# Performance work log

Hardware: AMD Instinct MI355X
Metric: run time of the kernel (lower is better)

Reference implementation:

```python
import jax, jax.numpy as jnp
import numpy as np

PAD = 1
THRESH = 10.0


def setup_inputs() -> dict:
    key = jax.random.key(0)
    k1, k2, k3 = jax.random.split(key, 3)
    x = jax.random.normal(k1, (8, 16, 62, 62), dtype=jnp.float32)
    W = jax.random.normal(k2, (32, 16, 3, 3), dtype=jnp.float32)
    b = jax.random.normal(k3, (32,), dtype=jnp.float32)
    return {"x": x, "W": W, "b": b}


def reference(x, W, b):
    # ZeroPad2d(padding) on all four sides
    x = jnp.pad(x, ((0, 0), (0, 0), (PAD, PAD), (PAD, PAD)))
    T, C, xr, xc = x.shape
    O, _, wr, wc = W.shape
    L = xr * xc

    # get_xfft_thresh: 1D FFT over flattened HxW, zero coeffs with |Re| < thresh
    xf = jnp.fft.fft(x.reshape(T, C, L))                      # (T,C,L) complex
    xf = jnp.where(jnp.abs(xf.real) < THRESH, jnp.zeros_like(xf), xf)

    # get_Wfft: zero-pad kernel to (xr,xc) bottom/right, flatten, reverse along
    # length (flipud(flip([0,1])) nets to a flip of the last axis only), then FFT
    Wp = jnp.pad(W, ((0, 0), (0, 0), (0, xr - wr), (0, xc - wc))).reshape(O, C, L)
    Wf = jnp.fft.fft(Wp[:, :, ::-1])                          # (O,C,L) complex

    # fftConv1D, batched over (image, out_channel):
    y = jnp.fft.ifft(xf[:, None, :, :] * Wf[None, :, :, :]).real  # (T,O,C,L)
    # torch.roll(y, 1) with no dims rolls the FLATTENED (C*L) tensor by 1
    y = jnp.roll(y.reshape(T, O, C * L), 1, axis=-1).reshape(T, O, C, xr, xc)
    y = y.sum(axis=2)                                         # sum over in-channels
    ans_r, ans_c = xr - wr + 1, xc - wc + 1
    y = y[:, :, :ans_r, :ans_c]
    return y + b[None, :, None, None]
```

## Files before the change

### kernel.cpp

```cpp
#include <hip/hip_runtime.h>
#include <math.h>

#define TWO_PI 6.28318530717958647692f
#define NT     1024
#define RPW    4
#define PITCH  65
#define THRESH 10.0f
#define C128   0.998795456205172393f
#define S128   0.049067674327418015f

typedef float v2f __attribute__((ext_vector_type(2)));

__device__ __forceinline__ int brev6(int x) {
    return (int)(__brev((unsigned)x) >> 26);
}

__device__ __forceinline__ v2f cmul_add(v2f a, v2f b, v2f acc) {
    acc += (v2f){a.x, a.x} * b;
    acc += (v2f){a.y, a.y} * (v2f){-b.y, b.x};
    return acc;
}

struct Tw6 { v2f t[6]; };

__device__ __forceinline__ Tw6 make_tw6(int lane, float sign) {
    Tw6 T;
    #pragma unroll
    for (int s = 0; s < 6; ++s) {
        int h = 1 << s;
        int j = lane & (h - 1);
        float ang = sign * (TWO_PI / 64.0f) * (float)(j * (32 >> s));
        float c, si;
        __sincosf(ang, &si, &c);
        T.t[s] = (v2f){c, si};
    }
    return T;
}

template<int R>
__device__ __forceinline__ void fft64_dif_t(float (&re)[R], float (&im)[R],
                                            int lane, const Tw6& T) {
    #pragma unroll
    for (int s = 5; s >= 0; --s) {
        const int h = 1 << s;
        float wr = T.t[s].x, wi = T.t[s].y;
        bool upper = (lane & h) != 0;
        float cwr = upper ? wr : 1.0f;
        float cwi = upper ? wi : 0.0f;
        float sgn = upper ? -1.0f : 1.0f;
        #pragma unroll
        for (int m = 0; m < R; ++m) {
            float orr = __shfl_xor(re[m], h, 64);
            float oii = __shfl_xor(im[m], h, 64);
            float ar = fmaf(sgn, re[m], orr);
            float ai = fmaf(sgn, im[m], oii);
            re[m] = ar * cwr - ai * cwi;
            im[m] = ar * cwi + ai * cwr;
        }
    }
}

template<int R>
__device__ __forceinline__ void fft64_dit_t(float (&re)[R], float (&im)[R],
                                            int lane, const Tw6& T) {
    #pragma unroll
    for (int s = 0; s < 6; ++s) {
        const int h = 1 << s;
        float wr = T.t[s].x, wi = T.t[s].y;
        bool upper = (lane & h) != 0;
        float cwr = upper ? wr : 1.0f;
        float cwi = upper ? wi : 0.0f;
        float sgn = upper ? -1.0f : 1.0f;
        #pragma unroll
        for (int m = 0; m < R; ++m) {
            float tr = re[m] * cwr - im[m] * cwi;
            float ti = re[m] * cwi + im[m] * cwr;
            float orr = __shfl_xor(tr, h, 64);
            float oii = __shfl_xor(ti, h, 64);
            re[m] = fmaf(sgn, tr, orr);
            im[m] = fmaf(sgn, ti, oii);
        }
    }
}

__global__ __launch_bounds__(NT) void fwd_kernel(const float* __restrict__ x,
                                                 float2* __restrict__ X) {
    __shared__ float sre[64 * PITCH];
    __shared__ float sim[64 * PITCH];
    const int task = blockIdx.x;
    const int tid  = threadIdx.x;
    const int lane = tid & 63;
    const int w    = tid >> 6;
    const float* xr = x + (size_t)task * 62 * 62;

    for (int idx = tid; idx < 4096; idx += NT) {
        int r = idx >> 6, s = idx & 63;
        float v = 0.0f;
        if (r >= 1 && r <= 62 && s >= 1 && s <= 62)
            v = xr[(r - 1) * 62 + (s - 1)];
        sre[r * PITCH + s] = v;
    }
    __syncthreads();

    const Tw6 Tf = make_tw6(lane, -1.0f);

    float re[RPW], im[RPW];
    #pragma unroll
    for (int m = 0; m < RPW; ++m) {
        re[m] = sre[lane * PITCH + (w * RPW + m)];
        im[m] = 0.0f;
    }
    fft64_dif_t<RPW>(re, im, lane, Tf);
    const int k1 = brev6(lane);
    #pragma unroll
    for (int m = 0; m < RPW; ++m) {
        int n2 = w * RPW + m;
        float cr, ci;
        __sincosf(-(TWO_PI / 4096.0f) * (float)(k1 * n2), &ci, &cr);
        float rr = re[m] * cr - im[m] * ci;
        im[m]    = re[m] * ci + im[m] * cr;
        re[m]    = rr;
    }
    __syncthreads();
    #pragma unroll
    for (int m = 0; m < RPW; ++m) {
        int n2 = w * RPW + m;
        sre[k1 * PITCH + n2] = re[m];
        sim[k1 * PITCH + n2] = im[m];
    }
    __syncthreads();

    float rb[3], ib[3];
    const int rows[3] = {2 * w, 2 * w + 1, 32};
    #pragma unroll
    for (int s = 0; s < 3; ++s) {
        rb[s] = sre[rows[s] * PITCH + lane];
        ib[s] = sim[rows[s] * PITCH + lane];
    }
    fft64_dif_t<3>(rb, ib, lane, Tf);
    float2* Xrow = X + (size_t)task * 4096;
    #pragma unroll
    for (int s = 0; s < 3; ++s) {
        if (s < 2 || w == 0) {
            float rr = rb[s], ii = ib[s];
            if (fabsf(rr) < THRESH) { rr = 0.0f; ii = 0.0f; }
            Xrow[rows[s] * 64 + lane] = make_float2(rr, ii);
        }
    }
}

__global__ __launch_bounds__(NT, 4) void conv_kernel(const float2* __restrict__ X,
                                                     const float* __restrict__ W,
                                                     const float* __restrict__ b,
                                                     float* __restrict__ out) {
    __shared__ float sre[64 * PITCH];
    __shared__ float sim[64 * PITCH];
    const int t    = blockIdx.x >> 5;
    const int o    = blockIdx.x & 31;
    const int tid  = threadIdx.x;
    const int lane = tid & 63;
    const int w    = tid >> 6;

    const int k2 = brev6(lane);
    float elr, eli;
    __sincosf((TWO_PI / 64.0f) * (float)k2, &eli, &elr);

    const Tw6 Ti = make_tw6(lane, +1.0f);

    const int rA = 2 * w, rB = 2 * w + 1;
    float uAr, uAi, vAr, vAi, uBr, uBi, vBr, vBi;
    __sincosf((TWO_PI / 64.0f) * (float)rA, &uAi, &uAr);
    __sincosf((TWO_PI / 4096.0f) * (float)rA, &vAi, &vAr);
    __sincosf((TWO_PI / 64.0f) * (float)rB, &uBi, &uBr);
    __sincosf((TWO_PI / 4096.0f) * (float)rB, &vBi, &vBr);
    v2f uA = {uAr, uAi};
    v2f vA = {vAr * elr - vAi * eli, vAr * eli + vAi * elr};
    v2f v2A = {vA.x * vA.x - vA.y * vA.y, 2.0f * vA.x * vA.y};
    v2f uB = {uBr, uBi};
    v2f vB = {vBr * elr - vBi * eli, vBr * eli + vBi * elr};
    v2f v2B = {vB.x * vB.x - vB.y * vB.y, 2.0f * vB.x * vB.y};
    v2f vC = {C128 * elr - S128 * eli, C128 * eli + S128 * elr};
    v2f v2C = {vC.x * vC.x - vC.y * vC.y, 2.0f * vC.x * vC.y};

    v2f SA = {0,0}, SB = {0,0}, SC = {0,0};

    const float2* Xt = X + (size_t)t * 16 * 4096 + lane;
    const float*  wo = W + o * 144;

    v2f xA[4], xB[4], xC[4];
    #pragma unroll
    for (int j = 0; j < 4; ++j) {
        { float2 q = Xt[j * 4096 + rA * 64]; xA[j] = (v2f){q.x, q.y}; }
        { float2 q = Xt[j * 4096 + rB * 64]; xB[j] = (v2f){q.x, q.y}; }
    }
    if (w == 0) {
        #pragma unroll
        for (int j = 0; j < 4; ++j) {
            float2 q = Xt[j * 4096 + 32 * 64]; xC[j] = (v2f){q.x, q.y};
        }
    }
    #pragma unroll 1
    for (int cc = 0; cc < 4; ++cc) {
        v2f nA[4], nB[4], nC[4];
        if (cc < 3) {
            const float2* xp = Xt + (cc + 1) * 4 * 4096;
            #pragma unroll
            for (int j = 0; j < 4; ++j) {
                { float2 q = xp[j * 4096 + rA * 64]; nA[j] = (v2f){q.x, q.y}; }
                { float2 q = xp[j * 4096 + rB * 64]; nB[j] = (v2f){q.x, q.y}; }
            }
            if (w == 0) {
                #pragma unroll
                for (int j = 0; j < 4; ++j) {
                    float2 q = xp[j * 4096 + 32 * 64]; nC[j] = (v2f){q.x, q.y};
                }
            }
        }
        #pragma unroll
        for (int j = 0; j < 4; ++j) {
            const float* wc = wo + (cc * 4 + j) * 9;
            const float wa0 = wc[0], wa1 = wc[1], wa2 = wc[2];
            const float wa3 = wc[3], wa4 = wc[4], wa5 = wc[5];
            const float wa6 = wc[6], wa7 = wc[7], wa8 = wc[8];
            {
                v2f h0 = (v2f){wa0, 0.0f}; h0 += vA * wa1; h0 += v2A * wa2;
                v2f h1 = (v2f){wa3, 0.0f}; h1 += vA * wa4; h1 += v2A * wa5;
                v2f h2 = (v2f){wa6, 0.0f}; h2 += vA * wa7; h2 += v2A * wa8;
                v2f P  = cmul_add(uA, cmul_add(uA, h2, h1), h0);
                SA = cmul_add(xA[j], P, SA);
            }
            {
                v2f h0 = (v2f){wa0, 0.0f}; h0 += vB * wa1; h0 += v2B * wa2;
                v2f h1 = (v2f){wa3, 0.0f}; h1 += vB * wa4; h1 += v2B * wa5;
                v2f h2 = (v2f){wa6, 0.0f}; h2 += vB * wa7; h2 += v2B * wa8;
                v2f P  = cmul_add(uB, cmul_add(uB, h2, h1), h0);
                SB = cmul_add(xB[j], P, SB);
            }
            if (w == 0) {
                v2f h0 = (v2f){wa0, 0.0f}; h0 += vC * wa1; h0 += v2C * wa2;
                v2f h1 = (v2f){wa3, 0.0f}; h1 += vC * wa4; h1 += v2C * wa5;
                v2f h2 = (v2f){wa6, 0.0f}; h2 += vC * wa7; h2 += v2C * wa8;
                v2f P  = h0 - h1 + h2;
                SC = cmul_add(xC[j], P, SC);
            }
        }
        #pragma unroll
        for (int j = 0; j < 4; ++j) { xA[j] = nA[j]; xB[j] = nB[j]; }
        if (w == 0) {
            #pragma unroll
            for (int j = 0; j < 4; ++j) xC[j] = nC[j];
        }
    }

    sre[rA * PITCH + k2] = SA.x; sim[rA * PITCH + k2] = SA.y;
    sre[rB * PITCH + k2] = SB.x; sim[rB * PITCH + k2] = SB.y;
    if (w == 0) { sre[32 * PITCH + k2] = SC.x; sim[32 * PITCH + k2] = SC.y; }
    __syncthreads();

    float re[RPW], im[RPW];
    #pragma unroll
    for (int m = 0; m < RPW; ++m) {
        int k1 = w * RPW + m;
        if (k1 <= 32) {
            re[m] = sre[k1 * PITCH + k2];
            im[m] = sim[k1 * PITCH + k2];
        } else {
            int k1p = 64 - k1, k2p = 63 - k2;
            re[m] =  sre[k1p * PITCH + k2p];
            im[m] = -sim[k1p * PITCH + k2p];
        }
    }
    __syncthreads();

    fft64_dit_t<RPW>(re, im, lane, Ti);
    {
        float cr, ci, sr, si;
        __sincosf((TWO_PI / 1024.0f) * (float)(lane * w), &ci, &cr);
        __sincosf((TWO_PI / 4096.0f) * (float)lane, &si, &sr);
        #pragma unroll
        for (int m = 0; m < RPW; ++m) {
            float rr = re[m] * cr - im[m] * ci;
            im[m]    = re[m] * ci + im[m] * cr;
            re[m]    = rr;
            float nr = cr * sr - ci * si;
            ci = cr * si + ci * sr; cr = nr;
        }
    }
    #pragma unroll
    for (int m = 0; m < RPW; ++m) {
        int k1 = w * RPW + m;
        sre[k1 * PITCH + lane] = re[m];
        sim[k1 * PITCH + lane] = im[m];
    }
    __syncthreads();
    #pragma unroll
    for (int m = 0; m < RPW; ++m) {
        int n2 = w * RPW + m;
        re[m] = sre[lane * PITCH + n2];
        im[m] = sim[lane * PITCH + n2];
    }
    fft64_dif_t<RPW>(re, im, lane, Ti);
    __syncthreads();
    const int n1 = brev6(lane);
    #pragma unroll
    for (int m = 0; m < RPW; ++m) {
        int n2 = w * RPW + m;
        sre[n1 * PITCH + n2] = re[m];
    }
    __syncthreads();
    const float bias = b[o];
    float* orow = out + (size_t)blockIdx.x * 62 * 62;
    for (int idx = tid; idx < 62 * 62; idx += NT) {
        int r = idx / 62, s = idx - r * 62;
        orow[idx] = sre[r * PITCH + s] * (1.0f / 4096.0f) + bias;
    }
}

extern "C" void kernel_launch(void* const* d_in, const int* in_sizes, int n_in,
                              void* d_out, int out_size, void* d_ws, size_t ws_size,
                              hipStream_t stream) {
    const float* x = (const float*)d_in[0];
    const float* W = (const float*)d_in[1];
    const float* b = (const float*)d_in[2];
    float* out = (float*)d_out;
    float2* X = (float2*)d_ws;

    fwd_kernel<<<dim3(128), dim3(NT), 0, stream>>>(x, X);
    conv_kernel<<<dim3(256), dim3(NT), 0, stream>>>(X, W, b, out);
}
```

Measured before the change: 82.07 us.

## Accumulate per-tap channel sums before applying twiddle polynomial in conv kernel

The conv kernel now first sums input spectra times each of the 9 real weights across all 16 channels, then applies the complex tap-position twiddle combination once per row. Before, it built the complex filter response per channel. This cuts per-channel complex arithmetic, but all 16 channel spectra are now loaded into registers at once instead of double-buffered in chunks of 4. Launch bounds drop from 4 to 3 blocks per CU to make room for the extra registers. The post-FFT twiddle now calls one sincos per element instead of using a recurrence.

```diff
diff --git a/kernel.cpp b/kernel.cpp
--- a/kernel.cpp
+++ b/kernel.cpp
@@ -81,6 +81,14 @@
             im[m] = fmaf(sgn, ti, oii);
         }
     }
+}
+
+__device__ __forceinline__ v2f tap_combine(const v2f (&T)[9], v2f u, v2f v,
+                                           v2f v2) {
+    v2f g0 = cmul_add(v2, T[2], cmul_add(v, T[1], T[0]));
+    v2f g1 = cmul_add(v2, T[5], cmul_add(v, T[4], T[3]));
+    v2f g2 = cmul_add(v2, T[8], cmul_add(v, T[7], T[6]));
+    return cmul_add(u, cmul_add(u, g2, g1), g0);
 }
 
 __global__ __launch_bounds__(NT) void fwd_kernel(const float* __restrict__ x,
@@ -149,7 +157,7 @@
     }
 }
 
-__global__ __launch_bounds__(NT, 4) void conv_kernel(const float2* __restrict__ X,
+__global__ __launch_bounds__(NT, 3) void conv_kernel(const float2* __restrict__ X,
                                                      const float* __restrict__ W,
                                                      const float* __restrict__ b,
                                                      float* __restrict__ out) {
@@ -179,82 +187,58 @@
     v2f uB = {uBr, uBi};
     v2f vB = {vBr * elr - vBi * eli, vBr * eli + vBi * elr};
     v2f v2B = {vB.x * vB.x - vB.y * vB.y, 2.0f * vB.x * vB.y};
-    v2f vC = {C128 * elr - S128 * eli, C128 * eli + S128 * elr};
-    v2f v2C = {vC.x * vC.x - vC.y * vC.y, 2.0f * vC.x * vC.y};
-
-    v2f SA = {0,0}, SB = {0,0}, SC = {0,0};
 
     const float2* Xt = X + (size_t)t * 16 * 4096 + lane;
     const float*  wo = W + o * 144;
 
-    v2f xA[4], xB[4], xC[4];
-    #pragma unroll
-    for (int j = 0; j < 4; ++j) {
-        { float2 q = Xt[j * 4096 + rA * 64]; xA[j] = (v2f){q.x, q.y}; }
-        { float2 q = Xt[j * 4096 + rB * 64]; xB[j] = (v2f){q.x, q.y}; }
-    }
-    if (w == 0) {
-        #pragma unroll
-        for (int j = 0; j < 4; ++j) {
-            float2 q = Xt[j * 4096 + 32 * 64]; xC[j] = (v2f){q.x, q.y};
-        }
-    }
-    #pragma unroll 1
-    for (int cc = 0; cc < 4; ++cc) {
-        v2f nA[4], nB[4], nC[4];
-        if (cc < 3) {
-            const float2* xp = Xt + (cc + 1) * 4 * 4096;
-            #pragma unroll
-            for (int j = 0; j < 4; ++j) {
-                { float2 q = xp[j * 4096 + rA * 64]; nA[j] = (v2f){q.x, q.y}; }
-                { float2 q = xp[j * 4096 + rB * 64]; nB[j] = (v2f){q.x, q.y}; }
-            }
-            if (w == 0) {
-                #pragma unroll
-                for (int j = 0; j < 4; ++j) {
-                    float2 q = xp[j * 4096 + 32 * 64]; nC[j] = (v2f){q.x, q.y};
-                }
-            }
-        }
-        #pragma unroll
-        for (int j = 0; j < 4; ++j) {
-            const float* wc = wo + (cc * 4 + j) * 9;
-            const float wa0 = wc[0], wa1 = wc[1], wa2 = wc[2];
-            const float wa3 = wc[3], wa4 = wc[4], wa5 = wc[5];
-            const float wa6 = wc[6], wa7 = wc[7], wa8 = wc[8];
-            {
-                v2f h0 = (v2f){wa0, 0.0f}; h0 += vA * wa1; h0 += v2A * wa2;
-                v2f h1 = (v2f){wa3, 0.0f}; h1 += vA * wa4; h1 += v2A * wa5;
-                v2f h2 = (v2f){wa6, 0.0f}; h2 += vA * wa7; h2 += v2A * wa8;
-                v2f P  = cmul_add(uA, cmul_add(uA, h2, h1), h0);
-                SA = cmul_add(xA[j], P, SA);
-            }
-            {
-                v2f h0 = (v2f){wa0, 0.0f}; h0 += vB * wa1; h0 += v2B * wa2;
-                v2f h1 = (v2f){wa3, 0.0f}; h1 += vB * wa4; h1 += v2B * wa5;
-                v2f h2 = (v2f){wa6, 0.0f}; h2 += vB * wa7; h2 += v2B * wa8;
-                v2f P  = cmul_add(uB, cmul_add(uB, h2, h1), h0);
-                SB = cmul_add(xB[j], P, SB);
-            }
-            if (w == 0) {
-                v2f h0 = (v2f){wa0, 0.0f}; h0 += vC * wa1; h0 += v2C * wa2;
-                v2f h1 = (v2f){wa3, 0.0f}; h1 += vC * wa4; h1 += v2C * wa5;
-                v2f h2 = (v2f){wa6, 0.0f}; h2 += vC * wa7; h2 += v2C * wa8;
-                v2f P  = h0 - h1 + h2;
-                SC = cmul_add(xC[j], P, SC);
-            }
-        }
-        #pragma unroll
-        for (int j = 0; j < 4; ++j) { xA[j] = nA[j]; xB[j] = nB[j]; }
-        if (w == 0) {
-            #pragma unroll
-            for (int j = 0; j < 4; ++j) xC[j] = nC[j];
-        }
-    }
+    v2f xA[16], xB[16];
+    #pragma unroll
+    for (int c = 0; c < 16; ++c) {
+        { float2 q = Xt[c * 4096 + rA * 64]; xA[c] = (v2f){q.x, q.y}; }
+        { float2 q = Xt[c * 4096 + rB * 64]; xB[c] = (v2f){q.x, q.y}; }
+    }
+    v2f TA[9], TB[9];
+    #pragma unroll
+    for (int q = 0; q < 9; ++q) { TA[q] = (v2f){0,0}; TB[q] = (v2f){0,0}; }
+    #pragma unroll
+    for (int c = 0; c < 16; ++c) {
+        const float* wc = wo + c * 9;
+        #pragma unroll
+        for (int q = 0; q < 9; ++q) {
+            float wq = wc[q];
+            TA[q] += xA[c] * wq;
+            TB[q] += xB[c] * wq;
+        }
+    }
+    v2f SA = tap_combine(TA, uA, vA, v2A);
+    v2f SB = tap_combine(TB, uB, vB, v2B);
 
     sre[rA * PITCH + k2] = SA.x; sim[rA * PITCH + k2] = SA.y;
     sre[rB * PITCH + k2] = SB.x; sim[rB * PITCH + k2] = SB.y;
-    if (w == 0) { sre[32 * PITCH + k2] = SC.x; sim[32 * PITCH + k2] = SC.y; }
+
+    if (w == 0) {
+        v2f xC[16];
+        #pragma unroll
+        for (int c = 0; c < 16; ++c) {
+            float2 q = Xt[c * 4096 + 32 * 64]; xC[c] = (v2f){q.x, q.y};
+        }
+        v2f TC[9];
+        #pragma unroll
+        for (int q = 0; q < 9; ++q) TC[q] = (v2f){0,0};
+        #pragma unroll
+        for (int c = 0; c < 16; ++c) {
+            const float* wc = wo + c * 9;
+            #pragma unroll
+            for (int q = 0; q < 9; ++q) TC[q] += xC[c] * wc[q];
+        }
+        v2f vC = {C128 * elr - S128 * eli, C128 * eli + S128 * elr};
+        v2f v2C = {vC.x * vC.x - vC.y * vC.y, 2.0f * vC.x * vC.y};
+        v2f g0 = cmul_add(v2C, TC[2], cmul_add(vC, TC[1], TC[0]));
+        v2f g1 = cmul_add(v2C, TC[5], cmul_add(vC, TC[4], TC[3]));
+        v2f g2 = cmul_add(v2C, TC[8], cmul_add(vC, TC[7], TC[6]));
+        v2f SC = g0 - g1 + g2;
+        sre[32 * PITCH + k2] = SC.x; sim[32 * PITCH + k2] = SC.y;
+    }
     __syncthreads();
 
     float re[RPW], im[RPW];
@@ -273,18 +257,14 @@
     __syncthreads();
 
     fft64_dit_t<RPW>(re, im, lane, Ti);
-    {
-        float cr, ci, sr, si;
-        __sincosf((TWO_PI / 1024.0f) * (float)(lane * w), &ci, &cr);
-        __sincosf((TWO_PI / 4096.0f) * (float)lane, &si, &sr);
-        #pragma unroll
-        for (int m = 0; m < RPW; ++m) {
-            float rr = re[m] * cr - im[m] * ci;
-            im[m]    = re[m] * ci + im[m] * cr;
-            re[m]    = rr;
-            float nr = cr * sr - ci * si;
-            ci = cr * si + ci * sr; cr = nr;
-        }
+    #pragma unroll
+    for (int m = 0; m < RPW; ++m) {
+        int k1 = w * RPW + m;
+        float cr, ci;
+        __sincosf((TWO_PI / 4096.0f) * (float)(lane * k1), &ci, &cr);
+        float rr = re[m] * cr - im[m] * ci;
+        im[m]    = re[m] * ci + im[m] * cr;
+        re[m]    = rr;
     }
     #pragma unroll
     for (int m = 0; m < RPW; ++m) {
```

Measured after the change: 79.52 us. 3.1% less time.
